# Performance work log

Hardware: AMD Instinct MI355X
Metric: run time of the kernel (lower is better)

## Reference

```python
import jax, jax.numpy as jnp
import numpy as np

N = 2_000_000
SH_C0 = 0.282095  # Y_0^0
SH_C1 = 0.488603  # Y_1^m


def setup_inputs() -> dict:
    key = jax.random.key(0)
    k1, k2, k3, k4 = jax.random.split(key, 4)
    positions = jax.random.normal(k1, (N, 3), dtype=jnp.float32)
    colors = jax.random.uniform(k2, (N, 3), dtype=jnp.float32)
    alphas = jnp.ones((N,), dtype=jnp.float32)
    R = jax.random.normal(k3, (N, 3, 3), dtype=jnp.float32)
    S = jax.random.normal(k4, (N, 3, 3), dtype=jnp.float32)
    return {"positions": positions, "colors": colors, "alphas": alphas, "R": R, "S": S}


def _sh_coeffs(colors):
    # colors: [N, 3] -> sh: [N, 4] (band-0 constant + band-1 scaled channels)
    l0 = jnp.full_like(colors[:, 0:1], SH_C0)
    l1_1 = colors[:, 1:2] * SH_C1
    l1_0 = colors[:, 0:1] * SH_C1
    l1_1n = colors[:, 2:3] * SH_C1
    return jnp.concatenate([l0, l1_1, l1_0, l1_1n], axis=1)


def reference(positions, colors, alphas, R, S):
    # Sigma = R (S S^T) R^T, per point, all [N,3,3]
    S_sq = jnp.einsum("nij,nkj->nik", S, S)          # S @ S^T
    cov = jnp.einsum("nij,njk,nlk->nil", R, S_sq, R)  # R @ S_sq @ R^T
    sh = _sh_coeffs(colors)
    return (positions, cov, alphas, sh)
```

## Files before the change

kernel.cpp:

```cpp
#include <hip/hip_runtime.h>


#define SH_C0 0.282095f
#define SH_C1 0.488603f
#define BLK 256
#define GRID 2048

__global__ __launch_bounds__(BLK) void gs_kernel(
    const float* __restrict__ pos,
    const float* __restrict__ col,
    const float* __restrict__ alp,
    const float* __restrict__ Rm,
    const float* __restrict__ Sm,
    float* __restrict__ out_pos,
    float* __restrict__ out_cov,
    float* __restrict__ out_alp,
    float* __restrict__ out_sh,
    int n)
{
    const int T = gridDim.x * blockDim.x;
    const int g = blockIdx.x * blockDim.x + threadIdx.x;

    {
        const int nf = 3 * n;
        const int n4 = nf >> 2;
        const float4* src = (const float4*)pos;
        float4* dst = (float4*)out_pos;
        for (int u = g; u < n4; u += T) dst[u] = src[u];
        for (int u = (n4 << 2) + g; u < nf; u += T) out_pos[u] = pos[u];
    }

    {
        const int n4 = n >> 2;
        const float4* src = (const float4*)alp;
        float4* dst = (float4*)out_alp;
        for (int u = g; u < n4; u += T) dst[u] = src[u];
        for (int u = (n4 << 2) + g; u < n; u += T) out_alp[u] = alp[u];
    }

    {
        float4* sh4 = (float4*)out_sh;
        for (int i = g; i < n; i += T) {
            float c0 = col[3 * i + 0];
            float c1 = col[3 * i + 1];
            float c2 = col[3 * i + 2];
            sh4[i] = make_float4(SH_C0, c1 * SH_C1, c0 * SH_C1, c2 * SH_C1);
        }
    }

    for (int i = g; i < n; i += T) {
        float r[9], s[9];
#pragma unroll
        for (int k = 0; k < 9; ++k) r[k] = Rm[9 * i + k];
#pragma unroll
        for (int k = 0; k < 9; ++k) s[k] = Sm[9 * i + k];

        float t[9];
#pragma unroll
        for (int a = 0; a < 3; ++a)
#pragma unroll
            for (int b = 0; b < 3; ++b)
                t[3 * a + b] = r[3 * a + 0] * s[0 + b]
                             + r[3 * a + 1] * s[3 + b]
                             + r[3 * a + 2] * s[6 + b];

#pragma unroll
        for (int a = 0; a < 3; ++a)
#pragma unroll
            for (int b = 0; b < 3; ++b)
                out_cov[9 * i + 3 * a + b] = t[3 * a + 0] * t[3 * b + 0]
                                           + t[3 * a + 1] * t[3 * b + 1]
                                           + t[3 * a + 2] * t[3 * b + 2];
    }
}

extern "C" void kernel_launch(void* const* d_in, const int* in_sizes, int n_in,
                              void* d_out, int out_size, void* d_ws, size_t ws_size,
                              hipStream_t stream) {
    const float* pos = (const float*)d_in[0];
    const float* col = (const float*)d_in[1];
    const float* alp = (const float*)d_in[2];
    const float* Rm  = (const float*)d_in[3];
    const float* Sm  = (const float*)d_in[4];

    int n = in_sizes[0] / 3;

    float* out = (float*)d_out;
    float* out_pos = out;
    float* out_cov = out + 3 * n;
    float* out_alp = out + 12 * n;
    float* out_sh  = out + 13 * n;

    gs_kernel<<<GRID, BLK, 0, stream>>>(pos, col, alp, Rm, Sm,
                                        out_pos, out_cov, out_alp, out_sh, n);
}
```

Measured before the change: 280.4 us.

## Stage AoS color, R, S and covariance tiles through LDS for coalesced float4 access

The per-point colour, R and S loads and the covariance stores now run tile by tile: each block loads 256 points of R and S into shared memory with float4 reads, computes from LDS, writes the covariance into LDS, then stores it back with float4 writes. The colour-to-SH path is staged through LDS the same way. This replaces strided scalar loads and stores on stride-9 and stride-3 layouts with fully coalesced vector transfers. In exchange it adds __syncthreads barriers, LDS traffic with possible bank conflicts at stride 9, and 27 KB of shared memory per block, which may limit occupancy.

```diff
diff --git a/kernel.cpp b/kernel.cpp
--- a/kernel.cpp
+++ b/kernel.cpp
@@ -18,8 +18,15 @@
     float* __restrict__ out_sh,
     int n)
 {
+    __shared__ float4 lds[1728];
+    float4* ldsR = lds;
+    float4* ldsS = lds + 576;
+    float4* ldsC = lds + 1152;
+
+    const int t = threadIdx.x;
     const int T = gridDim.x * blockDim.x;
-    const int g = blockIdx.x * blockDim.x + threadIdx.x;
+    const int g = blockIdx.x * blockDim.x + t;
+    const int full_tiles = n / BLK;
 
     {
         const int nf = 3 * n;
@@ -40,7 +47,17 @@
 
     {
         float4* sh4 = (float4*)out_sh;
-        for (int i = g; i < n; i += T) {
+        for (int tile = blockIdx.x; tile < full_tiles; tile += gridDim.x) {
+            const int base = tile * BLK;
+            const float4* C4 = (const float4*)(col + (size_t)base * 3);
+            if (t < 192) lds[t] = C4[t];
+            __syncthreads();
+            const float* cc = (const float*)lds + t * 3;
+            sh4[base + t] = make_float4(SH_C0, cc[1] * SH_C1,
+                                        cc[0] * SH_C1, cc[2] * SH_C1);
+            __syncthreads();
+        }
+        for (int i = full_tiles * BLK + g; i < n; i += T) {
             float c0 = col[3 * i + 0];
             float c1 = col[3 * i + 1];
             float c2 = col[3 * i + 2];
@@ -48,29 +65,76 @@
         }
     }
 
-    for (int i = g; i < n; i += T) {
+    for (int tile = blockIdx.x; tile < full_tiles; tile += gridDim.x) {
+        const int base = tile * BLK;
+        const float4* R4 = (const float4*)(Rm + (size_t)base * 9);
+        const float4* S4 = (const float4*)(Sm + (size_t)base * 9);
+        float4* OC4 = (float4*)(out_cov + (size_t)base * 9);
+
+        ldsR[t]       = R4[t];
+        ldsR[t + 256] = R4[t + 256];
+        ldsS[t]       = S4[t];
+        ldsS[t + 256] = S4[t + 256];
+        if (t < 64) {
+            ldsR[t + 512] = R4[t + 512];
+            ldsS[t + 512] = S4[t + 512];
+        }
+        __syncthreads();
+
+        const float* rf = (const float*)ldsR + t * 9;
+        const float* sf = (const float*)ldsS + t * 9;
+        float r[9], s[9];
+#pragma unroll
+        for (int k = 0; k < 9; ++k) r[k] = rf[k];
+#pragma unroll
+        for (int k = 0; k < 9; ++k) s[k] = sf[k];
+
+        float tm[9];
+#pragma unroll
+        for (int a = 0; a < 3; ++a)
+#pragma unroll
+            for (int b = 0; b < 3; ++b)
+                tm[3 * a + b] = r[3 * a + 0] * s[0 + b]
+                              + r[3 * a + 1] * s[3 + b]
+                              + r[3 * a + 2] * s[6 + b];
+
+        float* cf = (float*)ldsC + t * 9;
+#pragma unroll
+        for (int a = 0; a < 3; ++a)
+#pragma unroll
+            for (int b = 0; b < 3; ++b)
+                cf[3 * a + b] = tm[3 * a + 0] * tm[3 * b + 0]
+                              + tm[3 * a + 1] * tm[3 * b + 1]
+                              + tm[3 * a + 2] * tm[3 * b + 2];
+        __syncthreads();
+
+        OC4[t]       = ldsC[t];
+        OC4[t + 256] = ldsC[t + 256];
+        if (t < 64) OC4[t + 512] = ldsC[t + 512];
+    }
+    for (int i = full_tiles * BLK + g; i < n; i += T) {
         float r[9], s[9];
 #pragma unroll
         for (int k = 0; k < 9; ++k) r[k] = Rm[9 * i + k];
 #pragma unroll
         for (int k = 0; k < 9; ++k) s[k] = Sm[9 * i + k];
 
-        float t[9];
+        float tm[9];
 #pragma unroll
         for (int a = 0; a < 3; ++a)
 #pragma unroll
             for (int b = 0; b < 3; ++b)
-                t[3 * a + b] = r[3 * a + 0] * s[0 + b]
-                             + r[3 * a + 1] * s[3 + b]
-                             + r[3 * a + 2] * s[6 + b];
+                tm[3 * a + b] = r[3 * a + 0] * s[0 + b]
+                              + r[3 * a + 1] * s[3 + b]
+                              + r[3 * a + 2] * s[6 + b];
 
 #pragma unroll
         for (int a = 0; a < 3; ++a)
 #pragma unroll
             for (int b = 0; b < 3; ++b)
-                out_cov[9 * i + 3 * a + b] = t[3 * a + 0] * t[3 * b + 0]
-                                           + t[3 * a + 1] * t[3 * b + 1]
-                                           + t[3 * a + 2] * t[3 * b + 2];
+                out_cov[9 * i + 3 * a + b] = tm[3 * a + 0] * tm[3 * b + 0]
+                                           + tm[3 * a + 1] * tm[3 * b + 1]
+                                           + tm[3 * a + 2] * tm[3 * b + 2];
     }
 }
 
```

New measurement: 281.8 us. About the same (+0.5%).
